# Optimization experiments

Hardware: AMD Instinct MI355X
Metric: run time of the kernel (lower is better)

The kernel has to match this reference:

```python
import jax, jax.numpy as jnp
import numpy as np

B, N, C, H = 8, 1024, 1024, 16
HD = C // H
SCALE = HD ** -0.5

def setup_inputs() -> dict:
    key = jax.random.key(0)
    k1, k2, k3, k4 = jax.random.split(key, 4)
    x = jax.random.normal(k1, (B, N, C), dtype=jnp.float32)
    # torch nn.Linear weights: [out, in]
    w_qkv = jax.random.normal(k2, (3 * C, C), dtype=jnp.float32) * (C ** -0.5)
    w_proj = jax.random.normal(k3, (C, C), dtype=jnp.float32) * (C ** -0.5)
    b_proj = jax.random.normal(k4, (C,), dtype=jnp.float32) * 0.02
    return {"x": x, "w_qkv": w_qkv, "w_proj": w_proj, "b_proj": b_proj}

def reference(x, w_qkv, w_proj, b_proj):
    Bv, Nv, Cv = x.shape
    # qkv projection (no bias); torch Linear: x @ W^T
    qkv = jnp.einsum('bnc,dc->bnd', x, w_qkv)
    qkv = qkv.reshape(Bv, Nv, 3, H, HD).transpose(2, 0, 3, 1, 4)  # [3,B,H,N,hd]
    q, k, v = qkv[0], qkv[1], qkv[2]
    attn = jnp.einsum('bhnd,bhmd->bhnm', q, k) * SCALE  # [B,H,N,N]
    attn = jax.nn.softmax(attn, axis=-1)
    out = jnp.einsum('bhnm,bhmd->bhnd', attn, v)
    out = out.transpose(0, 2, 1, 3).reshape(Bv, Nv, Cv)
    out = jnp.einsum('bnc,dc->bnd', out, w_proj) + b_proj
    return out
```

## Files before the change

kernel.cpp:

```cpp
#include <hip/hip_runtime.h>


typedef __attribute__((ext_vector_type(8))) short bf16x8;
typedef __attribute__((ext_vector_type(4))) short bf16x4;
typedef __attribute__((ext_vector_type(4))) float f32x4;

__device__ __forceinline__ short f2bf(float f) {
    union { float f; unsigned u; } x;
    x.f = f;
    unsigned r = x.u + 0x7fffu + ((x.u >> 16) & 1u);
    return (short)(r >> 16);
}

__device__ __forceinline__ void load_lds16(const void* g, void* l) {
    __builtin_amdgcn_global_load_lds((const __attribute__((address_space(1))) unsigned*)g,
                                     (__attribute__((address_space(3))) unsigned*)l,
                                     16, 0, 0);
}

__global__ __launch_bounds__(256) void convert_all(const float* __restrict__ x,
                                                   const float* __restrict__ wqkv,
                                                   const float* __restrict__ wproj,
                                                   short* __restrict__ xb,
                                                   short* __restrict__ wqkvb,
                                                   short* __restrict__ wprojb) {
    int i = blockIdx.x * 256 + threadIdx.x;
    const float* src;
    short* dst;
    int j;
    if (i < 2097152)      { src = x;     dst = xb;     j = i; }
    else if (i < 2883584) { src = wqkv;  dst = wqkvb;  j = i - 2097152; }
    else                  { src = wproj; dst = wprojb; j = i - 2883584; }
    float4 v = *(const float4*)(src + j * 4);
    unsigned lo = (unsigned short)f2bf(v.x) | ((unsigned)(unsigned short)f2bf(v.y) << 16);
    unsigned hi = (unsigned short)f2bf(v.z) | ((unsigned)(unsigned short)f2bf(v.w) << 16);
    uint2 p; p.x = lo; p.y = hi;
    *(uint2*)(dst + j * 4) = p;
}

template<int EPI, int NTX>
__global__ __launch_bounds__(512, 2) void gemm256(const short* __restrict__ A,
                                                  const short* __restrict__ Bt,
                                                  short* __restrict__ q,
                                                  short* __restrict__ kk,
                                                  short* __restrict__ vt,
                                                  const float* __restrict__ bias,
                                                  float* __restrict__ out) {
    extern __shared__ short lds[];
    short* const As = lds;
    short* const Bs = lds + 32768;
    const int K = 1024;

    constexpr int CHUNK = NTX * 4;
    const int bid = blockIdx.x;
    const int tile = (bid & 7) * CHUNK + (bid >> 3);
    const int m0 = (tile / NTX) * 256;
    const int n0 = (tile % NTX) * 256;

    const int t = threadIdx.x;
    const int w = t >> 6, lane = t & 63, quad = lane >> 4, l16 = lane & 15;
    const int wm = (w >> 2) * 128, wn = (w & 3) * 64;
    const int sw = l16 & 7;

    const int srow = t >> 3;
    const int scol = ((t & 7) ^ (srow & 7)) * 8;
    const short* Ag = A  + (m0 + srow) * K + scol;
    const short* Bg = Bt + (n0 + srow) * K + scol;
    short* const Asw = As + (w * 8) * 64;
    short* const Bsw = Bs + (w * 8) * 64;

    f32x4 acc[8][4];
    #pragma unroll
    for (int mi = 0; mi < 8; ++mi)
        #pragma unroll
        for (int ni = 0; ni < 4; ++ni) acc[mi][ni] = (f32x4){0.f, 0.f, 0.f, 0.f};

    bf16x8 af[4][2], bf[4][2];

#define STG_A(kt_, d_, r_) load_lds16(Ag + (r_) * 64 * K + (kt_) * 64, Asw + (d_) * 16384 + (r_) * 4096)
#define STG_B(kt_, d_, r_) load_lds16(Bg + (r_) * 64 * K + (kt_) * 64, Bsw + (d_) * 16384 + (r_) * 4096)

    STG_A(0, 0, 0); STG_A(0, 0, 1); STG_A(0, 0, 2); STG_A(0, 0, 3);
    STG_B(0, 0, 0); STG_B(0, 0, 1); STG_B(0, 0, 2); STG_B(0, 0, 3);
    STG_A(1, 1, 0); STG_A(1, 1, 1); STG_A(1, 1, 2); STG_A(1, 1, 3);
    STG_B(1, 1, 0); STG_B(1, 1, 1); STG_B(1, 1, 2); STG_B(1, 1, 3);
    asm volatile("s_waitcnt vmcnt(8)" ::: "memory");
    asm volatile("s_barrier" ::: "memory");

    #pragma unroll
    for (int kt = 0; kt < 16; ++kt) {
        const int d = kt & 1;
        const short* Ar = As + d * 16384;
        const short* Br = Bs + d * 16384;

        #pragma unroll
        for (int mi = 0; mi < 4; ++mi)
            #pragma unroll
            for (int c = 0; c < 2; ++c)
                af[mi][c] = *(const bf16x8*)(Ar + (wm + mi * 16 + l16) * 64 + (((quad + 4 * c) ^ sw) * 8));
        #pragma unroll
        for (int ni = 0; ni < 2; ++ni)
            #pragma unroll
            for (int c = 0; c < 2; ++c)
                bf[ni][c] = *(const bf16x8*)(Br + (wn + ni * 16 + l16) * 64 + (((quad + 4 * c) ^ sw) * 8));
        asm volatile("s_barrier" ::: "memory");
        asm volatile("s_waitcnt lgkmcnt(0)" ::: "memory");
        __builtin_amdgcn_sched_barrier(0);
        __builtin_amdgcn_s_setprio(1);
        #pragma unroll
        for (int mi = 0; mi < 4; ++mi)
            #pragma unroll
            for (int ni = 0; ni < 2; ++ni) {
                acc[mi][ni] = __builtin_amdgcn_mfma_f32_16x16x32_bf16(af[mi][0], bf[ni][0], acc[mi][ni], 0, 0, 0);
                acc[mi][ni] = __builtin_amdgcn_mfma_f32_16x16x32_bf16(af[mi][1], bf[ni][1], acc[mi][ni], 0, 0, 0);
            }
        __builtin_amdgcn_s_setprio(0);
        asm volatile("s_barrier" ::: "memory");

        #pragma unroll
        for (int ni = 2; ni < 4; ++ni)
            #pragma unroll
            for (int c = 0; c < 2; ++c)
                bf[ni][c] = *(const bf16x8*)(Br + (wn + ni * 16 + l16) * 64 + (((quad + 4 * c) ^ sw) * 8));
        if (kt < 14) { STG_A(kt + 2, d, 0); STG_A(kt + 2, d, 2); }
        asm volatile("s_barrier" ::: "memory");
        asm volatile("s_waitcnt lgkmcnt(0)" ::: "memory");
        __builtin_amdgcn_sched_barrier(0);
        __builtin_amdgcn_s_setprio(1);
        #pragma unroll
        for (int mi = 0; mi < 4; ++mi)
            #pragma unroll
            for (int ni = 2; ni < 4; ++ni) {
                acc[mi][ni] = __builtin_amdgcn_mfma_f32_16x16x32_bf16(af[mi][0], bf[ni][0], acc[mi][ni], 0, 0, 0);
                acc[mi][ni] = __builtin_amdgcn_mfma_f32_16x16x32_bf16(af[mi][1], bf[ni][1], acc[mi][ni], 0, 0, 0);
            }
        __builtin_amdgcn_s_setprio(0);
        asm volatile("s_barrier" ::: "memory");

        #pragma unroll
        for (int mi = 0; mi < 4; ++mi)
            #pragma unroll
            for (int c = 0; c < 2; ++c)
                af[mi][c] = *(const bf16x8*)(Ar + (wm + 64 + mi * 16 + l16) * 64 + (((quad + 4 * c) ^ sw) * 8));
        if (kt < 14) { STG_B(kt + 2, d, 0); STG_B(kt + 2, d, 1); }
        asm volatile("s_barrier" ::: "memory");
        asm volatile("s_waitcnt lgkmcnt(0)" ::: "memory");
        __builtin_amdgcn_sched_barrier(0);
        __builtin_amdgcn_s_setprio(1);
        #pragma unroll
        for (int mi = 0; mi < 4; ++mi)
            #pragma unroll
            for (int ni = 0; ni < 2; ++ni) {
                acc[mi + 4][ni] = __builtin_amdgcn_mfma_f32_16x16x32_bf16(af[mi][0], bf[ni][0], acc[mi + 4][ni], 0, 0, 0);
                acc[mi + 4][ni] = __builtin_amdgcn_mfma_f32_16x16x32_bf16(af[mi][1], bf[ni][1], acc[mi + 4][ni], 0, 0, 0);
            }
        __builtin_amdgcn_s_setprio(0);
        asm volatile("s_barrier" ::: "memory");

        __builtin_amdgcn_s_setprio(1);
        #pragma unroll
        for (int mi = 0; mi < 4; ++mi)
            #pragma unroll
            for (int ni = 2; ni < 4; ++ni) {
                acc[mi + 4][ni] = __builtin_amdgcn_mfma_f32_16x16x32_bf16(af[mi][0], bf[ni][0], acc[mi + 4][ni], 0, 0, 0);
                acc[mi + 4][ni] = __builtin_amdgcn_mfma_f32_16x16x32_bf16(af[mi][1], bf[ni][1], acc[mi + 4][ni], 0, 0, 0);
            }
        __builtin_amdgcn_s_setprio(0);
        if (kt < 14) { STG_B(kt + 2, d, 2); STG_B(kt + 2, d, 3); STG_A(kt + 2, d, 1); STG_A(kt + 2, d, 3); }
        if (kt < 14)       asm volatile("s_waitcnt vmcnt(8)" ::: "memory");
        else if (kt == 14) asm volatile("s_waitcnt vmcnt(0)" ::: "memory");
        asm volatile("s_barrier" ::: "memory");
    }
#undef STG_A
#undef STG_B

    if (EPI == 0) {
        const float QS = 0.125f * 1.44269504088896f;
        #pragma unroll
        for (int ni = 0; ni < 4; ++ni) {
            int col = n0 + wn + ni * 16 + l16;
            int sect = col >> 10;
            int c = col & 1023;
            int h = c >> 6, dd = c & 63;
            #pragma unroll
            for (int mi = 0; mi < 8; ++mi) {
                #pragma unroll
                for (int r = 0; r < 4; ++r) {
                    int m = m0 + wm + mi * 16 + quad * 4 + r;
                    int b = m >> 10, i = m & 1023;
                    float v = acc[mi][ni][r];
                    if (sect == 0)      q[((b * 16 + h) * 1024 + i) * 64 + dd] = f2bf(v * QS);
                    else if (sect == 1) kk[((b * 16 + h) * 1024 + i) * 64 + dd] = f2bf(v);
                    else                vt[((b * 16 + h) * 64 + dd) * 1024 + i] = f2bf(v);
                }
            }
        }
    } else {
        #pragma unroll
        for (int ni = 0; ni < 4; ++ni) {
            int col = n0 + wn + ni * 16 + l16;
            float bv = bias[col];
            #pragma unroll
            for (int mi = 0; mi < 8; ++mi) {
                #pragma unroll
                for (int r = 0; r < 4; ++r) {
                    int m = m0 + wm + mi * 16 + quad * 4 + r;
                    out[m * 1024 + col] = acc[mi][ni][r] + bv;
                }
            }
        }
    }
}

__global__ __launch_bounds__(256) void attn_kernel(const short* __restrict__ q,
                                                   const short* __restrict__ k,
                                                   const short* __restrict__ vt,
                                                   short* __restrict__ ao) {
    __shared__ alignas(16) short Ks[2][64][72];
    __shared__ alignas(16) short Vs[2][64][72];

    const int bh = blockIdx.y, qt = blockIdx.x;
    const int t = threadIdx.x, w = t >> 6, lane = t & 63, quad = lane >> 4, l16 = lane & 15;
    const short* qg = q  + (bh * 1024 + qt * 128) * 64;
    const short* kg = k  + bh * 65536;
    const short* vg = vt + bh * 65536;

    bf16x8 qf[2][2];
    for (int mi = 0; mi < 2; ++mi) {
        const short* qr = qg + (w * 32 + mi * 16 + l16) * 64;
        qf[mi][0] = *(const bf16x8*)(qr + quad * 8);
        qf[mi][1] = *(const bf16x8*)(qr + 32 + quad * 8);
    }

    const int r0 = t >> 3,          c80 = (t & 7) * 8;
    const int r1 = (t + 256) >> 3,  c81 = c80;

    float rs[2] = {0.f, 0.f};
    f32x4 oaccT[2][4];
    for (int mi = 0; mi < 2; ++mi)
        for (int dt = 0; dt < 4; ++dt) oaccT[mi][dt] = (f32x4){0.f, 0.f, 0.f, 0.f};

    {
        float4 a = *(const float4*)&kg[r0 * 64 + c80];
        float4 b = *(const float4*)&kg[r1 * 64 + c81];
        float4 c = *(const float4*)&vg[r0 * 1024 + c80];
        float4 d = *(const float4*)&vg[r1 * 1024 + c81];
        *(float4*)&Ks[0][r0][c80] = a;  *(float4*)&Ks[0][r1][c81] = b;
        *(float4*)&Vs[0][r0][c80] = c;  *(float4*)&Vs[0][r1][c81] = d;
    }

    for (int jt = 0; jt < 16; ++jt) {
        const int cur = jt & 1;
        asm volatile("s_waitcnt lgkmcnt(0)" ::: "memory");
        asm volatile("s_barrier" ::: "memory");

        float4 kr0, kr1, vr0, vr1;
        if (jt < 15) {
            int jn = jt + 1;
            kr0 = *(const float4*)&kg[(jn * 64 + r0) * 64 + c80];
            kr1 = *(const float4*)&kg[(jn * 64 + r1) * 64 + c81];
            vr0 = *(const float4*)&vg[r0 * 1024 + jn * 64 + c80];
            vr1 = *(const float4*)&vg[r1 * 1024 + jn * 64 + c81];
        }

        for (int js = 0; js < 4; ++js) {
            bf16x8 kf0 = *(const bf16x8*)&Ks[cur][js * 16 + l16][quad * 8];
            bf16x8 kf1 = *(const bf16x8*)&Ks[cur][js * 16 + l16][32 + quad * 8];
            bf16x4 vtf[4];
            for (int dt = 0; dt < 4; ++dt)
                vtf[dt] = *(const bf16x4*)&Vs[cur][dt * 16 + l16][js * 16 + quad * 4];
            for (int mi = 0; mi < 2; ++mi) {
                f32x4 s = (f32x4){0.f, 0.f, 0.f, 0.f};
                s = __builtin_amdgcn_mfma_f32_16x16x32_bf16(kf0, qf[mi][0], s, 0, 0, 0);
                s = __builtin_amdgcn_mfma_f32_16x16x32_bf16(kf1, qf[mi][1], s, 0, 0, 0);
                bf16x4 pfrag;
                for (int r = 0; r < 4; ++r) {
                    float p = __builtin_amdgcn_exp2f(s[r]);
                    rs[mi] += p;
                    pfrag[r] = f2bf(p);
                }
                for (int dt = 0; dt < 4; ++dt)
                    oaccT[mi][dt] = __builtin_amdgcn_mfma_f32_16x16x16bf16_1k(
                        vtf[dt], pfrag, oaccT[mi][dt], 0, 0, 0);
            }
        }

        if (jt < 15) {
            const int nxt = cur ^ 1;
            *(float4*)&Ks[nxt][r0][c80] = kr0;  *(float4*)&Ks[nxt][r1][c81] = kr1;
            *(float4*)&Vs[nxt][r0][c80] = vr0;  *(float4*)&Vs[nxt][r1][c81] = vr1;
        }
    }

    for (int mi = 0; mi < 2; ++mi) {
        rs[mi] += __shfl_xor(rs[mi], 16, 64);
        rs[mi] += __shfl_xor(rs[mi], 32, 64);
    }

    const int b = bh >> 4, h = bh & 15;
    for (int mi = 0; mi < 2; ++mi) {
        float inv = 1.0f / rs[mi];
        int i = qt * 128 + w * 32 + mi * 16 + l16;
        short* aor = ao + (b * 1024 + i) * 1024 + h * 64;
        for (int dt = 0; dt < 4; ++dt) {
            bf16x4 o4;
            for (int r = 0; r < 4; ++r) o4[r] = f2bf(oaccT[mi][dt][r] * inv);
            *(bf16x4*)(aor + dt * 16 + quad * 4) = o4;
        }
    }
}

extern "C" void kernel_launch(void* const* d_in, const int* in_sizes, int n_in,
                              void* d_out, int out_size, void* d_ws, size_t ws_size,
                              hipStream_t stream) {
    const float* x      = (const float*)d_in[0];
    const float* w_qkv  = (const float*)d_in[1];
    const float* w_proj = (const float*)d_in[2];
    const float* b_proj = (const float*)d_in[3];
    float* out = (float*)d_out;

    char* ws = (char*)d_ws;
    short* xb     = (short*)(ws);
    short* wqkvb  = (short*)(ws + 16777216);
    short* wprojb = (short*)(ws + 23068672);
    short* qb     = (short*)(ws + 25165824);
    short* kb     = (short*)(ws + 41943040);
    short* vtb    = (short*)(ws + 58720256);
    short* aob    = (short*)(ws + 75497472);

    static bool s_init = false;
    if (!s_init) {
        hipFuncSetAttribute(reinterpret_cast<const void*>(&gemm256<0, 12>),
                            hipFuncAttributeMaxDynamicSharedMemorySize, 131072);
        hipFuncSetAttribute(reinterpret_cast<const void*>(&gemm256<1, 4>),
                            hipFuncAttributeMaxDynamicSharedMemorySize, 131072);
        s_init = true;
    }

    convert_all<<<12288, 256, 0, stream>>>(x, w_qkv, w_proj, xb, wqkvb, wprojb);
    gemm256<0, 12><<<384, 512, 131072, stream>>>(xb, wqkvb, qb, kb, vtb, nullptr, nullptr);
    attn_kernel<<<dim3(8, 128), 256, 0, stream>>>(qb, kb, vtb, aob);
    gemm256<1, 4><<<128, 512, 131072, stream>>>(aob, wprojb, nullptr, nullptr, nullptr, b_proj, out);
}
```

Measured before the change: 266.9 us.

## Templatize GEMM tile shape and simplify K-loop into two-phase pipeline

```diff
diff --git a/kernel.cpp b/kernel.cpp
--- a/kernel.cpp
+++ b/kernel.cpp
@@ -38,28 +38,32 @@
     *(uint2*)(dst + j * 4) = p;
 }
 
-template<int EPI, int NTX>
-__global__ __launch_bounds__(512, 2) void gemm256(const short* __restrict__ A,
-                                                  const short* __restrict__ Bt,
-                                                  short* __restrict__ q,
-                                                  short* __restrict__ kk,
-                                                  short* __restrict__ vt,
-                                                  const float* __restrict__ bias,
-                                                  float* __restrict__ out) {
+template<int EPI, int BM, int BN, int NTX>
+__global__ __launch_bounds__(512, 2) void gemm2p(const short* __restrict__ A,
+                                                 const short* __restrict__ Bt,
+                                                 short* __restrict__ q,
+                                                 short* __restrict__ kk,
+                                                 short* __restrict__ vt,
+                                                 const float* __restrict__ bias,
+                                                 float* __restrict__ out) {
     extern __shared__ short lds[];
+    constexpr int AU = BM / 64, BU = BN / 64, NLD = AU + BU;
+    constexpr int WM = BM / 2, WN = BN / 4;
+    constexpr int MF = WM / 16, NF = WN / 16, MF2 = MF / 2;
+    constexpr int NWG = (8192 / BM) * NTX;
+    constexpr int CHUNK = NWG / 8;
     short* const As = lds;
-    short* const Bs = lds + 32768;
+    short* const Bs = lds + 2 * BM * 64;
     const int K = 1024;
 
-    constexpr int CHUNK = NTX * 4;
     const int bid = blockIdx.x;
     const int tile = (bid & 7) * CHUNK + (bid >> 3);
-    const int m0 = (tile / NTX) * 256;
-    const int n0 = (tile % NTX) * 256;
+    const int m0 = (tile / NTX) * BM;
+    const int n0 = (tile % NTX) * BN;
 
     const int t = threadIdx.x;
     const int w = t >> 6, lane = t & 63, quad = lane >> 4, l16 = lane & 15;
-    const int wm = (w >> 2) * 128, wn = (w & 3) * 64;
+    const int wm = (w >> 2) * WM, wn = (w & 3) * WN;
     const int sw = l16 & 7;
 
     const int srow = t >> 3;
@@ -69,121 +73,102 @@
     short* const Asw = As + (w * 8) * 64;
     short* const Bsw = Bs + (w * 8) * 64;
 
-    f32x4 acc[8][4];
-    #pragma unroll
-    for (int mi = 0; mi < 8; ++mi)
-        #pragma unroll
-        for (int ni = 0; ni < 4; ++ni) acc[mi][ni] = (f32x4){0.f, 0.f, 0.f, 0.f};
-
-    bf16x8 af[4][2], bf[4][2];
-
-#define STG_A(kt_, d_, r_) load_lds16(Ag + (r_) * 64 * K + (kt_) * 64, Asw + (d_) * 16384 + (r_) * 4096)
-#define STG_B(kt_, d_, r_) load_lds16(Bg + (r_) * 64 * K + (kt_) * 64, Bsw + (d_) * 16384 + (r_) * 4096)
-
-    STG_A(0, 0, 0); STG_A(0, 0, 1); STG_A(0, 0, 2); STG_A(0, 0, 3);
-    STG_B(0, 0, 0); STG_B(0, 0, 1); STG_B(0, 0, 2); STG_B(0, 0, 3);
-    STG_A(1, 1, 0); STG_A(1, 1, 1); STG_A(1, 1, 2); STG_A(1, 1, 3);
-    STG_B(1, 1, 0); STG_B(1, 1, 1); STG_B(1, 1, 2); STG_B(1, 1, 3);
-    asm volatile("s_waitcnt vmcnt(8)" ::: "memory");
+    f32x4 acc[MF][NF];
+    #pragma unroll
+    for (int mi = 0; mi < MF; ++mi)
+        #pragma unroll
+        for (int ni = 0; ni < NF; ++ni) acc[mi][ni] = (f32x4){0.f, 0.f, 0.f, 0.f};
+
+    bf16x8 af[MF2][2], bf[NF][2];
+
+#define STG_A(kt_, r_) load_lds16(Ag + (r_) * 64 * K + (kt_) * 64, Asw + ((kt_) & 1) * (BM * 64) + (r_) * 4096)
+#define STG_B(kt_, r_) load_lds16(Bg + (r_) * 64 * K + (kt_) * 64, Bsw + ((kt_) & 1) * (BN * 64) + (r_) * 4096)
+#define WAIT_VM_NLD() do { if constexpr (NLD == 7) asm volatile("s_waitcnt vmcnt(7)" ::: "memory"); \
+                           else                    asm volatile("s_waitcnt vmcnt(6)" ::: "memory"); } while (0)
+
+    #pragma unroll
+    for (int r = 0; r < AU; ++r) STG_A(0, r);
+    #pragma unroll
+    for (int r = 0; r < BU; ++r) STG_B(0, r);
+    #pragma unroll
+    for (int r = 0; r < AU; ++r) STG_A(1, r);
+    #pragma unroll
+    for (int r = 0; r < BU; ++r) STG_B(1, r);
+    WAIT_VM_NLD();
     asm volatile("s_barrier" ::: "memory");
 
     #pragma unroll
     for (int kt = 0; kt < 16; ++kt) {
-        const int d = kt & 1;
-        const short* Ar = As + d * 16384;
-        const short* Br = Bs + d * 16384;
-
-        #pragma unroll
-        for (int mi = 0; mi < 4; ++mi)
+        const short* Ar = As + (kt & 1) * (BM * 64);
+        const short* Br = Bs + (kt & 1) * (BN * 64);
+
+        #pragma unroll
+        for (int mi = 0; mi < MF2; ++mi)
             #pragma unroll
             for (int c = 0; c < 2; ++c)
                 af[mi][c] = *(const bf16x8*)(Ar + (wm + mi * 16 + l16) * 64 + (((quad + 4 * c) ^ sw) * 8));
         #pragma unroll
-        for (int ni = 0; ni < 2; ++ni)
+        for (int ni = 0; ni < NF; ++ni)
             #pragma unroll
             for (int c = 0; c < 2; ++c)
                 bf[ni][c] = *(const bf16x8*)(Br + (wn + ni * 16 + l16) * 64 + (((quad + 4 * c) ^ sw) * 8));
-        asm volatile("s_barrier" ::: "memory");
         asm volatile("s_waitcnt lgkmcnt(0)" ::: "memory");
         __builtin_amdgcn_sched_barrier(0);
         __builtin_amdgcn_s_setprio(1);
         #pragma unroll
-        for (int mi = 0; mi < 4; ++mi)
-            #pragma unroll
-            for (int ni = 0; ni < 2; ++ni) {
+        for (int mi = 0; mi < MF2; ++mi)
+            #pragma unroll
+            for (int ni = 0; ni < NF; ++ni) {
                 acc[mi][ni] = __builtin_amdgcn_mfma_f32_16x16x32_bf16(af[mi][0], bf[ni][0], acc[mi][ni], 0, 0, 0);
                 acc[mi][ni] = __builtin_amdgcn_mfma_f32_16x16x32_bf16(af[mi][1], bf[ni][1], acc[mi][ni], 0, 0, 0);
             }
         __builtin_amdgcn_s_setprio(0);
-        asm volatile("s_barrier" ::: "memory");
-
-        #pragma unroll
-        for (int ni = 2; ni < 4; ++ni)
+
+        #pragma unroll
+        for (int mi = 0; mi < MF2; ++mi)
             #pragma unroll
             for (int c = 0; c < 2; ++c)
-                bf[ni][c] = *(const bf16x8*)(Br + (wn + ni * 16 + l16) * 64 + (((quad + 4 * c) ^ sw) * 8));
-        if (kt < 14) { STG_A(kt + 2, d, 0); STG_A(kt + 2, d, 2); }
-        asm volatile("s_barrier" ::: "memory");
+                af[mi][c] = *(const bf16x8*)(Ar + (wm + (MF2 + mi) * 16 + l16) * 64 + (((quad + 4 * c) ^ sw) * 8));
         asm volatile("s_waitcnt lgkmcnt(0)" ::: "memory");
         __builtin_amdgcn_sched_barrier(0);
         __builtin_amdgcn_s_setprio(1);
         #pragma unroll
-        for (int mi = 0; mi < 4; ++mi)
-            #pragma unroll
-            for (int ni = 2; ni < 4; ++ni) {
-                acc[mi][ni] = __builtin_amdgcn_mfma_f32_16x16x32_bf16(af[mi][0], bf[ni][0], acc[mi][ni], 0, 0, 0);
-                acc[mi][ni] = __builtin_amdgcn_mfma_f32_16x16x32_bf16(af[mi][1], bf[ni][1], acc[mi][ni], 0, 0, 0);
+        for (int mi = 0; mi < MF2; ++mi)
+            #pragma unroll
+            for (int ni = 0; ni < NF; ++ni) {
+                acc[MF2 + mi][ni] = __builtin_amdgcn_mfma_f32_16x16x32_bf16(af[mi][0], bf[ni][0], acc[MF2 + mi][ni], 0, 0, 0);
+                acc[MF2 + mi][ni] = __builtin_amdgcn_mfma_f32_16x16x32_bf16(af[mi][1], bf[ni][1], acc[MF2 + mi][ni], 0, 0, 0);
             }
         __builtin_amdgcn_s_setprio(0);
-        asm volatile("s_barrier" ::: "memory");
-
-        #pragma unroll
-        for (int mi = 0; mi < 4; ++mi)
-            #pragma unroll
-            for (int c = 0; c < 2; ++c)
-                af[mi][c] = *(const bf16x8*)(Ar + (wm + 64 + mi * 16 + l16) * 64 + (((quad + 4 * c) ^ sw) * 8));
-        if (kt < 14) { STG_B(kt + 2, d, 0); STG_B(kt + 2, d, 1); }
-        asm volatile("s_barrier" ::: "memory");
-        asm volatile("s_waitcnt lgkmcnt(0)" ::: "memory");
-        __builtin_amdgcn_sched_barrier(0);
-        __builtin_amdgcn_s_setprio(1);
-        #pragma unroll
-        for (int mi = 0; mi < 4; ++mi)
-            #pragma unroll
-            for (int ni = 0; ni < 2; ++ni) {
-                acc[mi + 4][ni] = __builtin_amdgcn_mfma_f32_16x16x32_bf16(af[mi][0], bf[ni][0], acc[mi + 4][ni], 0, 0, 0);
-                acc[mi + 4][ni] = __builtin_amdgcn_mfma_f32_16x16x32_bf16(af[mi][1], bf[ni][1], acc[mi + 4][ni], 0, 0, 0);
-            }
-        __builtin_amdgcn_s_setprio(0);
-        asm volatile("s_barrier" ::: "memory");
-
-        __builtin_amdgcn_s_setprio(1);
-        #pragma unroll
-        for (int mi = 0; mi < 4; ++mi)
-            #pragma unroll
-            for (int ni = 2; ni < 4; ++ni) {
-                acc[mi + 4][ni] = __builtin_amdgcn_mfma_f32_16x16x32_bf16(af[mi][0], bf[ni][0], acc[mi + 4][ni], 0, 0, 0);
-                acc[mi + 4][ni] = __builtin_amdgcn_mfma_f32_16x16x32_bf16(af[mi][1], bf[ni][1], acc[mi + 4][ni], 0, 0, 0);
-            }
-        __builtin_amdgcn_s_setprio(0);
-        if (kt < 14) { STG_B(kt + 2, d, 2); STG_B(kt + 2, d, 3); STG_A(kt + 2, d, 1); STG_A(kt + 2, d, 3); }
-        if (kt < 14)       asm volatile("s_waitcnt vmcnt(8)" ::: "memory");
-        else if (kt == 14) asm volatile("s_waitcnt vmcnt(0)" ::: "memory");
-        asm volatile("s_barrier" ::: "memory");
+
+        if (kt < 15) {
+            asm volatile("s_barrier" ::: "memory");
+            if (kt < 14) {
+                #pragma unroll
+                for (int r = 0; r < AU; ++r) STG_A(kt + 2, r);
+                #pragma unroll
+                for (int r = 0; r < BU; ++r) STG_B(kt + 2, r);
+                WAIT_VM_NLD();
+            } else {
+                asm volatile("s_waitcnt vmcnt(0)" ::: "memory");
+            }
+            asm volatile("s_barrier" ::: "memory");
+        }
     }
 #undef STG_A
 #undef STG_B
+#undef WAIT_VM_NLD
 
     if (EPI == 0) {
         const float QS = 0.125f * 1.44269504088896f;
         #pragma unroll
-        for (int ni = 0; ni < 4; ++ni) {
+        for (int ni = 0; ni < NF; ++ni) {
             int col = n0 + wn + ni * 16 + l16;
             int sect = col >> 10;
             int c = col & 1023;
             int h = c >> 6, dd = c & 63;
             #pragma unroll
-            for (int mi = 0; mi < 8; ++mi) {
+            for (int mi = 0; mi < MF; ++mi) {
                 #pragma unroll
                 for (int r = 0; r < 4; ++r) {
                     int m = m0 + wm + mi * 16 + quad * 4 + r;
@@ -197,11 +182,11 @@
         }
     } else {
         #pragma unroll
-        for (int ni = 0; ni < 4; ++ni) {
+        for (int ni = 0; ni < NF; ++ni) {
             int col = n0 + wn + ni * 16 + l16;
             float bv = bias[col];
             #pragma unroll
-            for (int mi = 0; mi < 8; ++mi) {
+            for (int mi = 0; mi < MF; ++mi) {
                 #pragma unroll
                 for (int r = 0; r < 4; ++r) {
                     int m = m0 + wm + mi * 16 + quad * 4 + r;
@@ -330,15 +315,15 @@
 
     static bool s_init = false;
     if (!s_init) {
-        hipFuncSetAttribute(reinterpret_cast<const void*>(&gemm256<0, 12>),
-                            hipFuncAttributeMaxDynamicSharedMemorySize, 131072);
-        hipFuncSetAttribute(reinterpret_cast<const void*>(&gemm256<1, 4>),
-                            hipFuncAttributeMaxDynamicSharedMemorySize, 131072);
+        hipFuncSetAttribute(reinterpret_cast<const void*>(&gemm2p<0, 256, 192, 16>),
+                            hipFuncAttributeMaxDynamicSharedMemorySize, 114688);
+        hipFuncSetAttribute(reinterpret_cast<const void*>(&gemm2p<1, 128, 256, 4>),
+                            hipFuncAttributeMaxDynamicSharedMemorySize, 98304);
         s_init = true;
     }
 
     convert_all<<<12288, 256, 0, stream>>>(x, w_qkv, w_proj, xb, wqkvb, wprojb);
-    gemm256<0, 12><<<384, 512, 131072, stream>>>(xb, wqkvb, qb, kb, vtb, nullptr, nullptr);
+    gemm2p<0, 256, 192, 16><<<512, 512, 114688, stream>>>(xb, wqkvb, qb, kb, vtb, nullptr, nullptr);
     attn_kernel<<<dim3(8, 128), 256, 0, stream>>>(qb, kb, vtb, aob);
-    gemm256<1, 4><<<128, 512, 131072, stream>>>(aob, wprojb, nullptr, nullptr, nullptr, b_proj, out);
-}
+    gemm2p<1, 128, 256, 4><<<256, 512, 98304, stream>>>(aob, wprojb, nullptr, nullptr, nullptr, b_proj, out);
+}
```

Result: faster. 256.5 us (-3.9%).
